# Optimization experiments

Hardware: AMD Instinct MI355X
Metric: run time of the kernel (lower is better)

The kernel has to match this reference:

```python
import jax, jax.numpy as jnp
import numpy as np

B, C1, C2, CF, H, W, NH = 1, 64, 256, 256, 64, 64, 8
HD = CF // NH
EPS = 1e-5


def setup_inputs() -> dict:
    key = jax.random.key(0)
    ks = jax.random.split(key, 12)
    s = 0.02
    return {
        "F_lidar": jax.random.normal(ks[0], (B, C1, H, W), jnp.float32),
        "F_cam": jax.random.normal(ks[1], (B, C2, H, W), jnp.float32),
        "Wq": jax.random.normal(ks[2], (CF, C1), jnp.float32) * s,
        "Wk": jax.random.normal(ks[3], (CF, C2), jnp.float32) * s,
        "Wv": jax.random.normal(ks[4], (CF, C2), jnp.float32) * s,
        "Wo": jax.random.normal(ks[5], (CF, CF), jnp.float32) * s,
        "Wres": jax.random.normal(ks[6], (CF, C1), jnp.float32) * s,
        "ln1_g": jnp.ones((CF,), jnp.float32),
        "ln1_b": jnp.zeros((CF,), jnp.float32),
        "ln2_g": jnp.ones((CF,), jnp.float32),
        "ln2_b": jnp.zeros((CF,), jnp.float32),
        "W1": jax.random.normal(ks[7], (4 * CF, CF), jnp.float32) * s,
        "b1": jnp.zeros((4 * CF,), jnp.float32),
        "W2": jax.random.normal(ks[8], (CF, 4 * CF), jnp.float32) * s,
        "b2": jnp.zeros((CF,), jnp.float32),
    }


def _ln(x, g, b):
    m = jnp.mean(x, axis=-1, keepdims=True)
    v = jnp.mean((x - m) ** 2, axis=-1, keepdims=True)
    return (x - m) * jax.lax.rsqrt(v + EPS) * g + b


def reference(F_lidar, F_cam, Wq, Wk, Wv, Wo, Wres, ln1_g, ln1_b, ln2_g, ln2_b, W1, b1, W2, b2):
    N = H * W
    # 1x1 convs == per-token linear projections on flattened tokens
    tok_l = F_lidar.reshape(B, C1, N).transpose(0, 2, 1)  # (B, N, C1)
    tok_c = F_cam.reshape(B, C2, N).transpose(0, 2, 1)    # (B, N, C2)
    Q = (tok_l @ Wq.T).reshape(B, N, NH, HD)
    K = (tok_c @ Wk.T).reshape(B, N, NH, HD)
    V = (tok_c @ Wv.T).reshape(B, N, NH, HD)
    scale = HD ** -0.5
    scores = jnp.einsum("bnhd,bmhd->bhnm", Q, K) * scale  # (B, NH, N, N)
    attn = jax.nn.softmax(scores, axis=-1)
    out = jnp.einsum("bhnm,bmhd->bnhd", attn, V).reshape(B, N, CF)
    out = out @ Wo.T                                      # out_proj (1x1 conv)
    res = tok_l @ Wres.T                                  # residual_proj
    x = _ln(res + out, ln1_g, ln1_b)
    # FFN (dropout is identity in eval)
    h = jax.nn.relu(x @ W1.T + b1)
    ffn = h @ W2.T + b2
    x = _ln(x + ffn, ln2_g, ln2_b)
    return x.transpose(0, 2, 1).reshape(B, CF, H, W)
```

## Files before the change

### kernel.cpp

```cpp
#include <hip/hip_runtime.h>
#include <math.h>

#define NTOK 4096
#define C1 64
#define C2 256
#define CF 256
#define NH 8
#define HD 32
#define CFF 1024
#define EPSF 1e-5f
#define SPLIT 4
#define KVBLK 128
#define QSCALE 0.25505654040876564f

using f32x4  = __attribute__((ext_vector_type(4))) float;
using bf16x8 = __attribute__((ext_vector_type(8))) short;
using u32x4  = __attribute__((ext_vector_type(4))) unsigned int;
typedef unsigned short ushort_t;

__device__ inline ushort_t f2bf(float x) {
    union { float f; unsigned int u; } v; v.f = x;
    unsigned int r = (v.u + 0x7FFFu + ((v.u >> 16) & 1u)) >> 16;
    return (ushort_t)r;
}
__device__ inline float bf2f(ushort_t u) {
    union { unsigned int i; float f; } v; v.i = ((unsigned int)u) << 16; return v.f;
}
__device__ inline unsigned int fbits(float x) {
    union { float f; unsigned int u; } v; v.f = x; return v.u;
}

__device__ inline float exp2_raw(float x) {
#if __has_builtin(__builtin_amdgcn_exp2f)
    return __builtin_amdgcn_exp2f(x);
#else
    float r;
    asm("v_exp_f32 %0, %1" : "=v"(r) : "v"(x));
    return r;
#endif
}

__global__ __launch_bounds__(256) void prep_kernel(
    const float* __restrict__ Wq, const float* __restrict__ Wk,
    const float* __restrict__ Wv, const float* __restrict__ Wo,
    const float* __restrict__ Wres, const float* __restrict__ W1,
    const float* __restrict__ W2, const float* __restrict__ F_lidar,
    const float* __restrict__ F_cam,
    ushort_t* oWq, ushort_t* oWk, ushort_t* oWv, ushort_t* oWo,
    ushort_t* oWres, ushort_t* oW1, ushort_t* oW2,
    ushort_t* __restrict__ Flt, ushort_t* __restrict__ Fct) {
    __shared__ float tls[32][33];
    int b = blockIdx.x;
    if (b < 736) {
        const float* src; ushort_t* dst; int base, lgK; bool tiled;
        if      (b < 16)  { src = Wq;   dst = oWq;   base = b;       lgK = 6;  tiled = false; }
        else if (b < 80)  { src = Wk;   dst = oWk;   base = b - 16;  lgK = 8;  tiled = false; }
        else if (b < 144) { src = Wv;   dst = oWv;   base = b - 80;  lgK = 8;  tiled = false; }
        else if (b < 208) { src = Wo;   dst = oWo;   base = b - 144; lgK = 8;  tiled = true; }
        else if (b < 224) { src = Wres; dst = oWres; base = b - 208; lgK = 6;  tiled = true; }
        else if (b < 480) { src = W1;   dst = oW1;   base = b - 224; lgK = 8;  tiled = true; }
        else              { src = W2;   dst = oW2;   base = b - 480; lgK = 10; tiled = true; }
        const int i = base * 1024 + threadIdx.x * 4;
        const float4 v = *(const float4*)(src + i);
        ushort4 pk;
        pk.x = f2bf(v.x); pk.y = f2bf(v.y); pk.z = f2bf(v.z); pk.w = f2bf(v.w);
        if (!tiled) {
            *(ushort4*)(dst + i) = pk;
        } else {
            const int c  = i >> lgK;
            const int kk = i & ((1 << lgK) - 1);
            const int tau = (c >> 8) * (1 << (lgK - 6)) + (kk >> 6);
            const int dst4 = tau * 16384 + (c & 255) * 64
                           + (((((kk >> 3) & 7)) ^ (c & 7)) << 3) + (kk & 7);
            *(ushort4*)(dst + dst4) = pk;
        }
        return;
    }
    b -= 736;
    const float* src; ushort_t* dst; int C, c0, n0;
    if (b < 256) { src = F_lidar; dst = Flt; C = C1; c0 = (b & 1) * 32; n0 = (b >> 1) * 32; }
    else { b -= 256; src = F_cam; dst = Fct; C = C2; c0 = (b & 7) * 32; n0 = (b >> 3) * 32; }
    const int tx = threadIdx.x & 31, ty = threadIdx.x >> 5;
#pragma unroll
    for (int i = 0; i < 32; i += 8) tls[ty + i][tx] = src[(size_t)(c0 + ty + i) * NTOK + n0 + tx];
    __syncthreads();
#pragma unroll
    for (int i = 0; i < 32; i += 8) dst[(size_t)(n0 + ty + i) * C + c0 + tx] = f2bf(tls[tx][ty + i]);
}

__global__ __launch_bounds__(256) void qkv_kernel(
    const ushort_t* __restrict__ Flt, const ushort_t* __restrict__ Fct,
    const ushort_t* __restrict__ Wqb, const ushort_t* __restrict__ Wkb,
    const ushort_t* __restrict__ Wvb,
    ushort_t* __restrict__ Qb, ushort_t* __restrict__ Kb, ushort_t* __restrict__ Vt) {
    const int z = blockIdx.z;
    const ushort_t* A = (z == 0) ? Flt : Fct;
    const ushort_t* W = (z == 0) ? Wqb : (z == 1) ? Wkb : Wvb;
    const int K = (z == 0) ? C1 : C2;

    const int tid = threadIdx.x;
    const int wid = tid >> 6, lane = tid & 63;
    const int g = lane >> 4, r = lane & 15;
    const int r0 = blockIdx.x * 128 + wid * 16;
    const int c0 = blockIdx.y * 64;

    f32x4 acc[2][4];
#pragma unroll
    for (int i = 0; i < 2; ++i)
#pragma unroll
        for (int t = 0; t < 4; ++t) acc[i][t] = (f32x4){0, 0, 0, 0};

    const ushort_t* ap0 = A + (size_t)(r0 + r) * K + (g << 3);
    const ushort_t* ap1 = ap0 + (size_t)64 * K;
    const ushort_t* wp = W + (size_t)(c0 + r) * K + (g << 3);
#pragma unroll 2
    for (int k0 = 0; k0 < K; k0 += 32) {
        const bf16x8 a0 = *(const bf16x8*)(ap0 + k0);
        const bf16x8 a1 = *(const bf16x8*)(ap1 + k0);
#pragma unroll
        for (int t = 0; t < 4; ++t) {
            const bf16x8 wf = *(const bf16x8*)(wp + (size_t)(t * 16) * K + k0);
            acc[0][t] = __builtin_amdgcn_mfma_f32_16x16x32_bf16(a0, wf, acc[0][t], 0, 0, 0);
            acc[1][t] = __builtin_amdgcn_mfma_f32_16x16x32_bf16(a1, wf, acc[1][t], 0, 0, 0);
        }
    }
    if (z == 0) {
#pragma unroll
        for (int i = 0; i < 2; ++i)
#pragma unroll
            for (int t = 0; t < 4; ++t) {
                const int col = c0 + 16 * t + r;
#pragma unroll
                for (int q = 0; q < 4; ++q)
                    Qb[(size_t)(r0 + i * 64 + 4 * g + q) * CF + col] = f2bf(acc[i][t][q] * QSCALE);
            }
    } else if (z == 1) {
#pragma unroll
        for (int i = 0; i < 2; ++i)
#pragma unroll
            for (int t = 0; t < 4; ++t) {
                const int col = c0 + 16 * t + r;
#pragma unroll
                for (int q = 0; q < 4; ++q) {
                    const int tok = r0 + i * 64 + 4 * g + q;
                    const int cs = (col & ~31) | ((((col >> 3) & 3) ^ ((tok >> 1) & 3)) << 3) | (col & 7);
                    Kb[(size_t)tok * CF + cs] = f2bf(acc[i][t][q]);
                }
            }
    } else {
#pragma unroll
        for (int i = 0; i < 2; ++i)
#pragma unroll
            for (int t = 0; t < 4; ++t) {
                const int dglob = c0 + 16 * t + r;
                const int hh = dglob >> 5, d = dglob & 31;
                const int tok0 = r0 + i * 64 + 4 * g;
                const int T = tok0 >> 7, tl = tok0 & 127;
                const int kc = tl >> 5, gp = (tl >> 2) & 3, jh = (tl >> 4) & 1;
                const int c = kc * 4 + gp;
                ushort4 pk;
                pk.x = f2bf(acc[i][t][0]); pk.y = f2bf(acc[i][t][1]);
                pk.z = f2bf(acc[i][t][2]); pk.w = f2bf(acc[i][t][3]);
                *(ushort4*)((char*)Vt + ((size_t)(hh * 32 + T) << 13)
                            + ((size_t)(c * 32 + (d ^ (c & 7))) << 4) + (jh << 3)) = pk;
            }
    }
}

__global__ __launch_bounds__(512, 4) void fattn_kernel(const ushort_t* __restrict__ Qb,
                                                       const ushort_t* __restrict__ Kb,
                                                       const ushort_t* __restrict__ Vt,
                                                       ushort_t* __restrict__ Opart,
                                                       float* __restrict__ Lst) {
    __shared__ ushort_t Ks[3][4096];
    __shared__ ushort_t Vs[3][4096];

    const int tid = threadIdx.x;
    const int wid = tid >> 6, lane = tid & 63;
    const int g = lane >> 4, r = lane & 15;
    const int bid = blockIdx.x;
    const int qb = bid & 15;
    const int sp = (bid >> 4) & (SPLIT - 1);
    const int h  = bid >> 6;
    const int n0 = qb * 256 + wid * 32;
    const int m_beg = sp * (NTOK / SPLIT);

    const bf16x8 qfA = *(const bf16x8*)(Qb + ((size_t)(n0 + r) << 8) + h * HD + (g << 3));
    const bf16x8 qfB = *(const bf16x8*)(Qb + ((size_t)(n0 + 16 + r) << 8) + h * HD + (g << 3));
    const bf16x8 onesf = {(short)0x3F80, (short)0x3F80, (short)0x3F80, (short)0x3F80,
                          (short)0x3F80, (short)0x3F80, (short)0x3F80, (short)0x3F80};

    const char* kb  = (const char*)Ks[0] + (r << 6) + ((g ^ ((r >> 1) & 3)) << 4);
    const char* vbg = (const char*)Vs[0] + (g << 9) + ((r & 8) << 4);
    const int slotbase = ((r & 7) ^ g) << 4;

    const int o = tid << 4;
    const char* ksrc = (const char*)Kb + (size_t)(m_beg + (o >> 6)) * 512 + (h << 6) + (o & 63);
    const char* vsrc = (const char*)Vt + ((size_t)(h * 32 + (m_beg >> 7)) << 13) + o;

    auto stage = [&](int bufs) {
        __builtin_amdgcn_global_load_lds(
            (const __attribute__((address_space(1))) unsigned int*)ksrc,
            (__attribute__((address_space(3))) unsigned int*)((char*)Ks[bufs] + (wid << 10)), 16, 0, 0);
        __builtin_amdgcn_global_load_lds(
            (const __attribute__((address_space(1))) unsigned int*)vsrc,
            (__attribute__((address_space(3))) unsigned int*)((char*)Vs[bufs] + (wid << 10)), 16, 0, 0);
        ksrc += KVBLK * 512;
        vsrc += 8192;
    };

    f32x4 accA0 = {0, 0, 0, 0}, accA1 = {0, 0, 0, 0}, laccA = {0, 0, 0, 0};
    f32x4 accB0 = {0, 0, 0, 0}, accB1 = {0, 0, 0, 0}, laccB = {0, 0, 0, 0};

    stage(0);
    stage(1);
    asm volatile("s_waitcnt vmcnt(2)" ::: "memory");
    __builtin_amdgcn_s_barrier();

    constexpr int NT = (NTOK / SPLIT) / KVBLK;
#pragma unroll
    for (int tt = 0; tt < NT; ++tt) {
        if (tt + 2 < NT) stage((tt + 2) % 3);
        const int bofs = (tt % 3) << 13;

        f32x4 sA[8], sB[8];
#pragma unroll
        for (int t8 = 0; t8 < 8; ++t8) {
            const bf16x8 kf = *(const bf16x8*)(kb + bofs + (t8 << 10));
            sA[t8] = __builtin_amdgcn_mfma_f32_16x16x32_bf16(kf, qfA, (f32x4){0, 0, 0, 0}, 0, 0, 0);
            sB[t8] = __builtin_amdgcn_mfma_f32_16x16x32_bf16(kf, qfB, (f32x4){0, 0, 0, 0}, 0, 0, 0);
        }
        u32x4 pkvA[4], pkvB[4];
#pragma unroll
        for (int t8 = 0; t8 < 8; ++t8) {
            const float a0 = exp2_raw(sA[t8][0]);
            const float a1 = exp2_raw(sA[t8][1]);
            const float a2 = exp2_raw(sA[t8][2]);
            const float a3 = exp2_raw(sA[t8][3]);
            pkvA[t8 >> 1][(t8 & 1) * 2]     = __builtin_amdgcn_perm(fbits(a1), fbits(a0), 0x07060302u);
            pkvA[t8 >> 1][(t8 & 1) * 2 + 1] = __builtin_amdgcn_perm(fbits(a3), fbits(a2), 0x07060302u);
        }
#pragma unroll
        for (int t8 = 0; t8 < 8; ++t8) {
            const float b0 = exp2_raw(sB[t8][0]);
            const float b1 = exp2_raw(sB[t8][1]);
            const float b2 = exp2_raw(sB[t8][2]);
            const float b3 = exp2_raw(sB[t8][3]);
            pkvB[t8 >> 1][(t8 & 1) * 2]     = __builtin_amdgcn_perm(fbits(b1), fbits(b0), 0x07060302u);
            pkvB[t8 >> 1][(t8 & 1) * 2 + 1] = __builtin_amdgcn_perm(fbits(b3), fbits(b2), 0x07060302u);
        }
#pragma unroll
        for (int kc = 0; kc < 4; ++kc) {
            union { u32x4 u; bf16x8 b; } puA, puB;
            puA.u = pkvA[kc]; puB.u = pkvB[kc];
            const bf16x8 pfA = puA.b, pfB = puB.b;
            laccA = __builtin_amdgcn_mfma_f32_16x16x32_bf16(pfA, onesf, laccA, 0, 0, 0);
            laccB = __builtin_amdgcn_mfma_f32_16x16x32_bf16(pfB, onesf, laccB, 0, 0, 0);
            const char* va = vbg + bofs + (kc << 11) + (slotbase ^ ((kc & 1) << 6));
            const bf16x8 vf0 = *(const bf16x8*)(va);
            const bf16x8 vf1 = *(const bf16x8*)(va + 256);
            accA0 = __builtin_amdgcn_mfma_f32_16x16x32_bf16(pfA, vf0, accA0, 0, 0, 0);
            accB0 = __builtin_amdgcn_mfma_f32_16x16x32_bf16(pfB, vf0, accB0, 0, 0, 0);
            accA1 = __builtin_amdgcn_mfma_f32_16x16x32_bf16(pfA, vf1, accA1, 0, 0, 0);
            accB1 = __builtin_amdgcn_mfma_f32_16x16x32_bf16(pfB, vf1, accB1, 0, 0, 0);
        }
        if (tt + 2 < NT) { asm volatile("s_waitcnt vmcnt(2)" ::: "memory"); }
        else             { asm volatile("s_waitcnt vmcnt(0)" ::: "memory"); }
        __builtin_amdgcn_s_barrier();
    }
    const size_t baseA = (size_t)(sp * NH + h) * NTOK + n0;
    const size_t baseB = baseA + 16;
    if (r == 0) {
        *(f32x4*)(Lst + baseA + 4 * g) = laccA;
        *(f32x4*)(Lst + baseB + 4 * g) = laccB;
    }
#pragma unroll
    for (int q = 0; q < 4; ++q) {
        const size_t rowbA = (baseA + 4 * g + q) * HD;
        Opart[rowbA + r]      = f2bf(accA0[q]);
        Opart[rowbA + 16 + r] = f2bf(accA1[q]);
        const size_t rowbB = (baseB + 4 * g + q) * HD;
        Opart[rowbB + r]      = f2bf(accB0[q]);
        Opart[rowbB + 16 + r] = f2bf(accB1[q]);
    }
}

__global__ __launch_bounds__(512) void tail_kernel(
    const ushort_t* __restrict__ Opart, const float* __restrict__ Lst,
    const ushort_t* __restrict__ Wo,
    const ushort_t* __restrict__ Flt, const ushort_t* __restrict__ Wres,
    const float* __restrict__ g1, const float* __restrict__ bt1,
    const ushort_t* __restrict__ W1, const float* __restrict__ b1,
    const ushort_t* __restrict__ W2, const float* __restrict__ b2,
    const float* __restrict__ g2, const float* __restrict__ bt2,
    float* __restrict__ out) {
    __shared__ ushort_t Wb[3][16384];
    __shared__ ushort_t As[16][264];
    __shared__ ushort_t Xs[16][264];
    __shared__ ushort_t Hs[16][1032];
    __shared__ float redS[8][16], redQ[8][16];
    const int tid = threadIdx.x;
    const int wid = tid >> 6, lane = tid & 63;
    const int g = lane >> 4, r = lane & 15;
    const int row0 = blockIdx.x * 16;
    const int cw = wid * 32;

    const ushort_t* ap2 = Flt + (size_t)(row0 + r) * C1 + (g << 3);
    const bf16x8 afl0 = *(const bf16x8*)(ap2);
    const bf16x8 afl1 = *(const bf16x8*)(ap2 + 32);

    const int wl00 = (cw + r) * 128 + ((g ^ (r & 7)) << 4);
    const int wl01 = wl00 + 2048;
    const int wl10 = (cw + r) * 128 + (((4 + g) ^ (r & 7)) << 4);
    const int wl11 = wl10 + 2048;

    auto stageW = [&](const ushort_t* src, int buf) {
        const char* s = (const char*)src + (tid << 4);
        char* d = (char*)&Wb[buf][0] + (tid << 4);
#pragma unroll
        for (int j = 0; j < 4; ++j) {
            __builtin_amdgcn_global_load_lds(
                (const __attribute__((address_space(1))) unsigned int*)(s + j * 8192),
                (__attribute__((address_space(3))) unsigned int*)(d + j * 8192), 16, 0, 0);
        }
    };

    {
        const int ri = tid >> 5;
        const int cc = (tid & 31) << 3;
        const int h  = cc >> 5, d0 = cc & 31;
        const int n  = row0 + ri;
        float L = 0.f;
#pragma unroll
        for (int s = 0; s < SPLIT; ++s) L += Lst[(size_t)(s * NH + h) * NTOK + n];
        const float invL = 1.f / L;
        float o[8] = {0.f, 0.f, 0.f, 0.f, 0.f, 0.f, 0.f, 0.f};
#pragma unroll
        for (int s = 0; s < SPLIT; ++s) {
            const ushort_t* p = Opart + ((size_t)(s * NH + h) * NTOK + n) * HD + d0;
            const ushort4 a = *(const ushort4*)p;
            const ushort4 b = *(const ushort4*)(p + 4);
            o[0] += bf2f(a.x); o[1] += bf2f(a.y); o[2] += bf2f(a.z); o[3] += bf2f(a.w);
            o[4] += bf2f(b.x); o[5] += bf2f(b.y); o[6] += bf2f(b.z); o[7] += bf2f(b.w);
        }
        ushort4 m0, m1;
        m0.x = f2bf(o[0] * invL); m0.y = f2bf(o[1] * invL);
        m0.z = f2bf(o[2] * invL); m0.w = f2bf(o[3] * invL);
        m1.x = f2bf(o[4] * invL); m1.y = f2bf(o[5] * invL);
        m1.z = f2bf(o[6] * invL); m1.w = f2bf(o[7] * invL);
        *(ushort4*)&As[ri][cc]     = m0;
        *(ushort4*)&As[ri][cc + 4] = m1;
    }
    __syncthreads();

    f32x4 accB[2] = {{0, 0, 0, 0}, {0, 0, 0, 0}};
    {
        stageW(Wo, 0);
        stageW(Wo + 16384, 1);
        asm volatile("s_waitcnt vmcnt(4)" ::: "memory");
        __builtin_amdgcn_s_barrier();
#pragma unroll
        for (int t = 0; t < 5; ++t) {
            if (t + 2 < 5) stageW(t + 2 < 4 ? Wo + (t + 2) * 16384 : Wres, (t + 2) % 3);
            const char* wb = (const char*)&Wb[t % 3][0];
            const bf16x8 w00 = *(const bf16x8*)(wb + wl00);
            const bf16x8 w01 = *(const bf16x8*)(wb + wl01);
            const bf16x8 w10 = *(const bf16x8*)(wb + wl10);
            const bf16x8 w11 = *(const bf16x8*)(wb + wl11);
            bf16x8 af0, af1;
            if (t < 4) {
                af0 = *(const bf16x8*)&As[r][t * 64 + (g << 3)];
                af1 = *(const bf16x8*)&As[r][t * 64 + 32 + (g << 3)];
            } else {
                af0 = afl0; af1 = afl1;
            }
            accB[0] = __builtin_amdgcn_mfma_f32_16x16x32_bf16(af0, w00, accB[0], 0, 0, 0);
            accB[1] = __builtin_amdgcn_mfma_f32_16x16x32_bf16(af0, w01, accB[1], 0, 0, 0);
            accB[0] = __builtin_amdgcn_mfma_f32_16x16x32_bf16(af1, w10, accB[0], 0, 0, 0);
            accB[1] = __builtin_amdgcn_mfma_f32_16x16x32_bf16(af1, w11, accB[1], 0, 0, 0);
            if (t + 2 < 5) { asm volatile("s_waitcnt vmcnt(4)" ::: "memory"); }
            else           { asm volatile("s_waitcnt vmcnt(0)" ::: "memory"); }
            __builtin_amdgcn_s_barrier();
        }
    }
    f32x4 xv[2];
    {
        f32x4 sv, qv;
#pragma unroll
        for (int q = 0; q < 4; ++q) {
            float s = accB[0][q] + accB[1][q];
            float sq = fmaf(accB[0][q], accB[0][q], accB[1][q] * accB[1][q]);
            s += __shfl_xor(s, 1); s += __shfl_xor(s, 2); s += __shfl_xor(s, 4); s += __shfl_xor(s, 8);
            sq += __shfl_xor(sq, 1); sq += __shfl_xor(sq, 2); sq += __shfl_xor(sq, 4); sq += __shfl_xor(sq, 8);
            sv[q] = s; qv[q] = sq;
        }
        if (r == 0) { *(f32x4*)&redS[wid][4 * g] = sv; *(f32x4*)&redQ[wid][4 * g] = qv; }
        __syncthreads();
        f32x4 S = {0, 0, 0, 0}, SQ = {0, 0, 0, 0};
#pragma unroll
        for (int w = 0; w < 8; ++w) {
            S  += *(const f32x4*)&redS[w][4 * g];
            SQ += *(const f32x4*)&redQ[w][4 * g];
        }
        f32x4 mn4, rs4;
#pragma unroll
        for (int q = 0; q < 4; ++q) {
            mn4[q] = S[q] * (1.f / CF);
            rs4[q] = rsqrtf(fmaxf(SQ[q] * (1.f / CF) - mn4[q] * mn4[q], 0.f) + EPSF);
        }
#pragma unroll
        for (int t = 0; t < 2; ++t) {
            const int col = cw + 16 * t + r;
            const float gam = g1[col], bet = bt1[col];
#pragma unroll
            for (int q = 0; q < 4; ++q) {
                xv[t][q] = (accB[t][q] - mn4[q]) * rs4[q] * gam + bet;
                Xs[4 * g + q][col] = f2bf(xv[t][q]);
            }
        }
    }
    __syncthreads();

    {
        f32x4 acc1[8];
#pragma unroll
        for (int t = 0; t < 8; ++t) acc1[t] = (f32x4){0, 0, 0, 0};
        stageW(W1, 0);
        stageW(W1 + 16384, 1);
        asm volatile("s_waitcnt vmcnt(4)" ::: "memory");
        __builtin_amdgcn_s_barrier();
#pragma unroll
        for (int t = 0; t < 16; ++t) {
            if (t + 2 < 16) stageW(W1 + (size_t)(t + 2) * 16384, (t + 2) % 3);
            const char* wb = (const char*)&Wb[t % 3][0];
            const bf16x8 w00 = *(const bf16x8*)(wb + wl00);
            const bf16x8 w01 = *(const bf16x8*)(wb + wl01);
            const bf16x8 w10 = *(const bf16x8*)(wb + wl10);
            const bf16x8 w11 = *(const bf16x8*)(wb + wl11);
            const bf16x8 af0 = *(const bf16x8*)&Xs[r][(t & 3) * 64 + (g << 3)];
            const bf16x8 af1 = *(const bf16x8*)&Xs[r][(t & 3) * 64 + 32 + (g << 3)];
            const int idx = (t >> 2) * 2;
            acc1[idx]     = __builtin_amdgcn_mfma_f32_16x16x32_bf16(w00, af0, acc1[idx], 0, 0, 0);
            acc1[idx + 1] = __builtin_amdgcn_mfma_f32_16x16x32_bf16(w01, af0, acc1[idx + 1], 0, 0, 0);
            acc1[idx]     = __builtin_amdgcn_mfma_f32_16x16x32_bf16(w10, af1, acc1[idx], 0, 0, 0);
            acc1[idx + 1] = __builtin_amdgcn_mfma_f32_16x16x32_bf16(w11, af1, acc1[idx + 1], 0, 0, 0);
            if (t + 2 < 16) { asm volatile("s_waitcnt vmcnt(4)" ::: "memory"); }
            else            { asm volatile("s_waitcnt vmcnt(0)" ::: "memory"); }
            __builtin_amdgcn_s_barrier();
        }
#pragma unroll
        for (int idx = 0; idx < 8; ++idx) {
            const int colb = (idx >> 1) * 256 + cw + 16 * (idx & 1) + 4 * g;
            const f32x4 bv = *(const f32x4*)(b1 + colb);
            ushort4 hw;
            hw.x = f2bf(fmaxf(acc1[idx][0] + bv[0], 0.f));
            hw.y = f2bf(fmaxf(acc1[idx][1] + bv[1], 0.f));
            hw.z = f2bf(fmaxf(acc1[idx][2] + bv[2], 0.f));
            hw.w = f2bf(fmaxf(acc1[idx][3] + bv[3], 0.f));
            *(ushort4*)&Hs[r][colb] = hw;
        }
    }

    f32x4 accD[2] = {{0, 0, 0, 0}, {0, 0, 0, 0}};
    {
        stageW(W2, 0);
        stageW(W2 + 16384, 1);
        asm volatile("s_waitcnt vmcnt(4)" ::: "memory");
        __builtin_amdgcn_s_barrier();
#pragma unroll
        for (int t = 0; t < 16; ++t) {
            if (t + 2 < 16) stageW(W2 + (size_t)(t + 2) * 16384, (t + 2) % 3);
            const char* wb = (const char*)&Wb[t % 3][0];
            const bf16x8 w00 = *(const bf16x8*)(wb + wl00);
            const bf16x8 w01 = *(const bf16x8*)(wb + wl01);
            const bf16x8 w10 = *(const bf16x8*)(wb + wl10);
            const bf16x8 w11 = *(const bf16x8*)(wb + wl11);
            const bf16x8 af0 = *(const bf16x8*)&Hs[r][t * 64 + (g << 3)];
            const bf16x8 af1 = *(const bf16x8*)&Hs[r][t * 64 + 32 + (g << 3)];
            accD[0] = __builtin_amdgcn_mfma_f32_16x16x32_bf16(af0, w00, accD[0], 0, 0, 0);
            accD[1] = __builtin_amdgcn_mfma_f32_16x16x32_bf16(af0, w01, accD[1], 0, 0, 0);
            accD[0] = __builtin_amdgcn_mfma_f32_16x16x32_bf16(af1, w10, accD[0], 0, 0, 0);
            accD[1] = __builtin_amdgcn_mfma_f32_16x16x32_bf16(af1, w11, accD[1], 0, 0, 0);
            if (t + 2 < 16) { asm volatile("s_waitcnt vmcnt(4)" ::: "memory"); }
            else            { asm volatile("s_waitcnt vmcnt(0)" ::: "memory"); }
            __builtin_amdgcn_s_barrier();
        }
    }
    {
#pragma unroll
        for (int t = 0; t < 2; ++t) {
            const float bb = b2[cw + 16 * t + r];
#pragma unroll
            for (int q = 0; q < 4; ++q) accD[t][q] += bb + xv[t][q];
        }
        f32x4 sv, qv;
#pragma unroll
        for (int q = 0; q < 4; ++q) {
            float s = accD[0][q] + accD[1][q];
            float sq = fmaf(accD[0][q], accD[0][q], accD[1][q] * accD[1][q]);
            s += __shfl_xor(s, 1); s += __shfl_xor(s, 2); s += __shfl_xor(s, 4); s += __shfl_xor(s, 8);
            sq += __shfl_xor(sq, 1); sq += __shfl_xor(sq, 2); sq += __shfl_xor(sq, 4); sq += __shfl_xor(sq, 8);
            sv[q] = s; qv[q] = sq;
        }
        if (r == 0) { *(f32x4*)&redS[wid][4 * g] = sv; *(f32x4*)&redQ[wid][4 * g] = qv; }
        __syncthreads();
        f32x4 S = {0, 0, 0, 0}, SQ = {0, 0, 0, 0};
#pragma unroll
        for (int w = 0; w < 8; ++w) {
            S  += *(const f32x4*)&redS[w][4 * g];
            SQ += *(const f32x4*)&redQ[w][4 * g];
        }
        f32x4 mn4, rs4;
#pragma unroll
        for (int q = 0; q < 4; ++q) {
            mn4[q] = S[q] * (1.f / CF);
            rs4[q] = rsqrtf(fmaxf(SQ[q] * (1.f / CF) - mn4[q] * mn4[q], 0.f) + EPSF);
        }
#pragma unroll
        for (int t = 0; t < 2; ++t) {
            const int col = cw + 16 * t + r;
            const float gam = g2[col], bet = bt2[col];
            f32x4 ov;
#pragma unroll
            for (int q = 0; q < 4; ++q)
                ov[q] = (accD[t][q] - mn4[q]) * rs4[q] * gam + bet;
            *(f32x4*)(out + (size_t)col * NTOK + row0 + 4 * g) = ov;
        }
    }
}

extern "C" void kernel_launch(void* const* d_in, const int* in_sizes, int n_in,
                              void* d_out, int out_size, void* d_ws, size_t ws_size,
                              hipStream_t stream) {
    const float* F_lidar = (const float*)d_in[0];
    const float* F_cam   = (const float*)d_in[1];
    const float* Wq      = (const float*)d_in[2];
    const float* Wk      = (const float*)d_in[3];
    const float* Wv      = (const float*)d_in[4];
    const float* Wo      = (const float*)d_in[5];
    const float* Wres    = (const float*)d_in[6];
    const float* ln1_g   = (const float*)d_in[7];
    const float* ln1_b   = (const float*)d_in[8];
    const float* ln2_g   = (const float*)d_in[9];
    const float* ln2_b   = (const float*)d_in[10];
    const float* W1      = (const float*)d_in[11];
    const float* b1      = (const float*)d_in[12];
    const float* W2      = (const float*)d_in[13];
    const float* b2      = (const float*)d_in[14];
    float* out = (float*)d_out;
    char* ws = (char*)d_ws;

    const size_t KB = 1024, MB = 1024 * 1024;
    ushort_t* Wq_b   = (ushort_t*)(ws + 0);
    ushort_t* Wk_b   = (ushort_t*)(ws + 32 * KB);
    ushort_t* Wv_b   = (ushort_t*)(ws + 160 * KB);
    ushort_t* Wo_b   = (ushort_t*)(ws + 288 * KB);
    ushort_t* Wres_b = (ushort_t*)(ws + 416 * KB);
    ushort_t* W1_b   = (ushort_t*)(ws + 448 * KB);
    ushort_t* W2_b   = (ushort_t*)(ws + 960 * KB);
    ushort_t* Flt    = (ushort_t*)(ws + 1536 * KB);
    ushort_t* Fct    = (ushort_t*)(ws + 2 * MB);
    ushort_t* Qb     = (ushort_t*)(ws + 4 * MB);
    ushort_t* Kb     = (ushort_t*)(ws + 6 * MB);
    ushort_t* Vt     = (ushort_t*)(ws + 8 * MB);
    ushort_t* Opart  = (ushort_t*)(ws + 12 * MB);
    float*    Lst    = (float*)(ws + 20 * MB);

    prep_kernel<<<2016, 256, 0, stream>>>(Wq, Wk, Wv, Wo, Wres, W1, W2, F_lidar, F_cam,
                                          Wq_b, Wk_b, Wv_b, Wo_b, Wres_b, W1_b, W2_b, Flt, Fct);
    qkv_kernel<<<dim3(NTOK / 128, CF / 64, 3), 256, 0, stream>>>(Flt, Fct, Wq_b, Wk_b, Wv_b, Qb, Kb, Vt);
    fattn_kernel<<<NH * SPLIT * (NTOK / 256), 512, 0, stream>>>(Qb, Kb, Vt, Opart, Lst);
    tail_kernel<<<NTOK / 16, 512, 0, stream>>>(Opart, Lst, Wo_b, Flt, Wres_b, ln1_g, ln1_b,
                                               W1_b, b1, W2_b, b2, ln2_g, ln2_b, out);
}
```

Baseline: 68.03 us.

## Unify tail weight streaming into one continuous pipeline and add MFMA priority hints

The tail kernel now streams Wo, Wres, W1 and W2 through a single triple-buffered LDS pipeline indexed by a global stage counter. Weight loads for the next GEMM are prefetched while the previous GEMM and its layernorm epilogue run, which removes the pipeline drain and refill between phases. LayerNorm and bias vectors and the lidar tile are also staged into LDS up front, and the attention kernel wraps its MFMA sections with s_setprio so waves issuing matrix work get scheduling priority. The cost is more LDS use per block and an extra __syncthreads between the FFN phases.

```diff
diff --git a/kernel.cpp b/kernel.cpp
--- a/kernel.cpp
+++ b/kernel.cpp
@@ -224,12 +224,14 @@
         const int bofs = (tt % 3) << 13;
 
         f32x4 sA[8], sB[8];
+        __builtin_amdgcn_s_setprio(1);
 #pragma unroll
         for (int t8 = 0; t8 < 8; ++t8) {
             const bf16x8 kf = *(const bf16x8*)(kb + bofs + (t8 << 10));
             sA[t8] = __builtin_amdgcn_mfma_f32_16x16x32_bf16(kf, qfA, (f32x4){0, 0, 0, 0}, 0, 0, 0);
             sB[t8] = __builtin_amdgcn_mfma_f32_16x16x32_bf16(kf, qfB, (f32x4){0, 0, 0, 0}, 0, 0, 0);
         }
+        __builtin_amdgcn_s_setprio(0);
         u32x4 pkvA[4], pkvB[4];
 #pragma unroll
         for (int t8 = 0; t8 < 8; ++t8) {
@@ -249,6 +251,7 @@
             pkvB[t8 >> 1][(t8 & 1) * 2]     = __builtin_amdgcn_perm(fbits(b1), fbits(b0), 0x07060302u);
             pkvB[t8 >> 1][(t8 & 1) * 2 + 1] = __builtin_amdgcn_perm(fbits(b3), fbits(b2), 0x07060302u);
         }
+        __builtin_amdgcn_s_setprio(1);
 #pragma unroll
         for (int kc = 0; kc < 4; ++kc) {
             union { u32x4 u; bf16x8 b; } puA, puB;
@@ -264,6 +267,7 @@
             accA1 = __builtin_amdgcn_mfma_f32_16x16x32_bf16(pfA, vf1, accA1, 0, 0, 0);
             accB1 = __builtin_amdgcn_mfma_f32_16x16x32_bf16(pfB, vf1, accB1, 0, 0, 0);
         }
+        __builtin_amdgcn_s_setprio(0);
         if (tt + 2 < NT) { asm volatile("s_waitcnt vmcnt(2)" ::: "memory"); }
         else             { asm volatile("s_waitcnt vmcnt(0)" ::: "memory"); }
         __builtin_amdgcn_s_barrier();
@@ -298,6 +302,8 @@
     __shared__ ushort_t As[16][264];
     __shared__ ushort_t Xs[16][264];
     __shared__ ushort_t Hs[16][1032];
+    __shared__ ushort_t Fs[16][72];
+    __shared__ float Bias[2304];
     __shared__ float redS[8][16], redQ[8][16];
     const int tid = threadIdx.x;
     const int wid = tid >> 6, lane = tid & 63;
@@ -305,10 +311,6 @@
     const int row0 = blockIdx.x * 16;
     const int cw = wid * 32;
 
-    const ushort_t* ap2 = Flt + (size_t)(row0 + r) * C1 + (g << 3);
-    const bf16x8 afl0 = *(const bf16x8*)(ap2);
-    const bf16x8 afl1 = *(const bf16x8*)(ap2 + 32);
-
     const int wl00 = (cw + r) * 128 + ((g ^ (r & 7)) << 4);
     const int wl01 = wl00 + 2048;
     const int wl10 = (cw + r) * 128 + (((4 + g) ^ (r & 7)) << 4);
@@ -323,6 +325,12 @@
                 (const __attribute__((address_space(1))) unsigned int*)(s + j * 8192),
                 (__attribute__((address_space(3))) unsigned int*)(d + j * 8192), 16, 0, 0);
         }
+    };
+    auto wsrc = [&](int s) -> const ushort_t* {
+        if (s < 4)  return Wo + (size_t)s * 16384;
+        if (s == 4) return Wres;
+        if (s < 21) return W1 + (size_t)(s - 5) * 16384;
+        return W2 + (size_t)(s - 21) * 16384;
     };
 
     {
@@ -350,38 +358,53 @@
         m1.z = f2bf(o[6] * invL); m1.w = f2bf(o[7] * invL);
         *(ushort4*)&As[ri][cc]     = m0;
         *(ushort4*)&As[ri][cc + 4] = m1;
+        *(ushort2*)&Fs[ri][(tid & 31) * 2] =
+            *(const ushort2*)(Flt + (size_t)(row0 + ri) * C1 + (tid & 31) * 2);
+#pragma unroll
+        for (int i5 = 0; i5 < 5; ++i5) {
+            const int i = i5 * 512 + tid;
+            if (i < 2304) {
+                float v;
+                if      (i < 256)  v = g1[i];
+                else if (i < 512)  v = bt1[i - 256];
+                else if (i < 768)  v = b2[i - 512];
+                else if (i < 1024) v = g2[i - 768];
+                else if (i < 1280) v = bt2[i - 1024];
+                else               v = b1[i - 1280];
+                Bias[i] = v;
+            }
+        }
     }
     __syncthreads();
 
+    stageW(wsrc(0), 0);
+    stageW(wsrc(1), 1);
+    asm volatile("s_waitcnt vmcnt(4)" ::: "memory");
+    __builtin_amdgcn_s_barrier();
+
     f32x4 accB[2] = {{0, 0, 0, 0}, {0, 0, 0, 0}};
-    {
-        stageW(Wo, 0);
-        stageW(Wo + 16384, 1);
+#pragma unroll
+    for (int t = 0; t < 5; ++t) {
+        stageW(wsrc(t + 2), (t + 2) % 3);
+        const char* wb = (const char*)&Wb[t % 3][0];
+        const bf16x8 w00 = *(const bf16x8*)(wb + wl00);
+        const bf16x8 w01 = *(const bf16x8*)(wb + wl01);
+        const bf16x8 w10 = *(const bf16x8*)(wb + wl10);
+        const bf16x8 w11 = *(const bf16x8*)(wb + wl11);
+        bf16x8 af0, af1;
+        if (t < 4) {
+            af0 = *(const bf16x8*)&As[r][t * 64 + (g << 3)];
+            af1 = *(const bf16x8*)&As[r][t * 64 + 32 + (g << 3)];
+        } else {
+            af0 = *(const bf16x8*)&Fs[r][(g << 3)];
+            af1 = *(const bf16x8*)&Fs[r][32 + (g << 3)];
+        }
+        accB[0] = __builtin_amdgcn_mfma_f32_16x16x32_bf16(af0, w00, accB[0], 0, 0, 0);
+        accB[1] = __builtin_amdgcn_mfma_f32_16x16x32_bf16(af0, w01, accB[1], 0, 0, 0);
+        accB[0] = __builtin_amdgcn_mfma_f32_16x16x32_bf16(af1, w10, accB[0], 0, 0, 0);
+        accB[1] = __builtin_amdgcn_mfma_f32_16x16x32_bf16(af1, w11, accB[1], 0, 0, 0);
         asm volatile("s_waitcnt vmcnt(4)" ::: "memory");
         __builtin_amdgcn_s_barrier();
-#pragma unroll
-        for (int t = 0; t < 5; ++t) {
-            if (t + 2 < 5) stageW(t + 2 < 4 ? Wo + (t + 2) * 16384 : Wres, (t + 2) % 3);
-            const char* wb = (const char*)&Wb[t % 3][0];
-            const bf16x8 w00 = *(const bf16x8*)(wb + wl00);
-            const bf16x8 w01 = *(const bf16x8*)(wb + wl01);
-            const bf16x8 w10 = *(const bf16x8*)(wb + wl10);
-            const bf16x8 w11 = *(const bf16x8*)(wb + wl11);
-            bf16x8 af0, af1;
-            if (t < 4) {
-                af0 = *(const bf16x8*)&As[r][t * 64 + (g << 3)];
-                af1 = *(const bf16x8*)&As[r][t * 64 + 32 + (g << 3)];
-            } else {
-                af0 = afl0; af1 = afl1;
-            }
-            accB[0] = __builtin_amdgcn_mfma_f32_16x16x32_bf16(af0, w00, accB[0], 0, 0, 0);
-            accB[1] = __builtin_amdgcn_mfma_f32_16x16x32_bf16(af0, w01, accB[1], 0, 0, 0);
-            accB[0] = __builtin_amdgcn_mfma_f32_16x16x32_bf16(af1, w10, accB[0], 0, 0, 0);
-            accB[1] = __builtin_amdgcn_mfma_f32_16x16x32_bf16(af1, w11, accB[1], 0, 0, 0);
-            if (t + 2 < 5) { asm volatile("s_waitcnt vmcnt(4)" ::: "memory"); }
-            else           { asm volatile("s_waitcnt vmcnt(0)" ::: "memory"); }
-            __builtin_amdgcn_s_barrier();
-        }
     }
     f32x4 xv[2];
     {
@@ -411,7 +434,7 @@
 #pragma unroll
         for (int t = 0; t < 2; ++t) {
             const int col = cw + 16 * t + r;
-            const float gam = g1[col], bet = bt1[col];
+            const float gam = Bias[col], bet = Bias[256 + col];
 #pragma unroll
             for (int q = 0; q < 4; ++q) {
                 xv[t][q] = (accB[t][q] - mn4[q]) * rs4[q] * gam + bet;
@@ -425,33 +448,29 @@
         f32x4 acc1[8];
 #pragma unroll
         for (int t = 0; t < 8; ++t) acc1[t] = (f32x4){0, 0, 0, 0};
-        stageW(W1, 0);
-        stageW(W1 + 16384, 1);
-        asm volatile("s_waitcnt vmcnt(4)" ::: "memory");
-        __builtin_amdgcn_s_barrier();
-#pragma unroll
-        for (int t = 0; t < 16; ++t) {
-            if (t + 2 < 16) stageW(W1 + (size_t)(t + 2) * 16384, (t + 2) % 3);
+#pragma unroll
+        for (int t = 5; t < 21; ++t) {
+            stageW(wsrc(t + 2), (t + 2) % 3);
+            const int tc = t - 5;
             const char* wb = (const char*)&Wb[t % 3][0];
             const bf16x8 w00 = *(const bf16x8*)(wb + wl00);
             const bf16x8 w01 = *(const bf16x8*)(wb + wl01);
             const bf16x8 w10 = *(const bf16x8*)(wb + wl10);
             const bf16x8 w11 = *(const bf16x8*)(wb + wl11);
-            const bf16x8 af0 = *(const bf16x8*)&Xs[r][(t & 3) * 64 + (g << 3)];
-            const bf16x8 af1 = *(const bf16x8*)&Xs[r][(t & 3) * 64 + 32 + (g << 3)];
-            const int idx = (t >> 2) * 2;
+            const bf16x8 af0 = *(const bf16x8*)&Xs[r][(tc & 3) * 64 + (g << 3)];
+            const bf16x8 af1 = *(const bf16x8*)&Xs[r][(tc & 3) * 64 + 32 + (g << 3)];
+            const int idx = (tc >> 2) * 2;
             acc1[idx]     = __builtin_amdgcn_mfma_f32_16x16x32_bf16(w00, af0, acc1[idx], 0, 0, 0);
             acc1[idx + 1] = __builtin_amdgcn_mfma_f32_16x16x32_bf16(w01, af0, acc1[idx + 1], 0, 0, 0);
             acc1[idx]     = __builtin_amdgcn_mfma_f32_16x16x32_bf16(w10, af1, acc1[idx], 0, 0, 0);
             acc1[idx + 1] = __builtin_amdgcn_mfma_f32_16x16x32_bf16(w11, af1, acc1[idx + 1], 0, 0, 0);
-            if (t + 2 < 16) { asm volatile("s_waitcnt vmcnt(4)" ::: "memory"); }
-            else            { asm volatile("s_waitcnt vmcnt(0)" ::: "memory"); }
+            asm volatile("s_waitcnt vmcnt(4)" ::: "memory");
             __builtin_amdgcn_s_barrier();
         }
 #pragma unroll
         for (int idx = 0; idx < 8; ++idx) {
             const int colb = (idx >> 1) * 256 + cw + 16 * (idx & 1) + 4 * g;
-            const f32x4 bv = *(const f32x4*)(b1 + colb);
+            const f32x4 bv = *(const f32x4*)&Bias[1280 + colb];
             ushort4 hw;
             hw.x = f2bf(fmaxf(acc1[idx][0] + bv[0], 0.f));
             hw.y = f2bf(fmaxf(acc1[idx][1] + bv[1], 0.f));
@@ -460,36 +479,32 @@
             *(ushort4*)&Hs[r][colb] = hw;
         }
     }
+    __syncthreads();
 
     f32x4 accD[2] = {{0, 0, 0, 0}, {0, 0, 0, 0}};
+#pragma unroll
+    for (int t = 21; t < 37; ++t) {
+        if (t + 2 < 37) stageW(wsrc(t + 2), (t + 2) % 3);
+        const int tc = t - 21;
+        const char* wb = (const char*)&Wb[t % 3][0];
+        const bf16x8 w00 = *(const bf16x8*)(wb + wl00);
+        const bf16x8 w01 = *(const bf16x8*)(wb + wl01);
+        const bf16x8 w10 = *(const bf16x8*)(wb + wl10);
+        const bf16x8 w11 = *(const bf16x8*)(wb + wl11);
+        const bf16x8 af0 = *(const bf16x8*)&Hs[r][tc * 64 + (g << 3)];
+        const bf16x8 af1 = *(const bf16x8*)&Hs[r][tc * 64 + 32 + (g << 3)];
+        accD[0] = __builtin_amdgcn_mfma_f32_16x16x32_bf16(af0, w00, accD[0], 0, 0, 0);
+        accD[1] = __builtin_amdgcn_mfma_f32_16x16x32_bf16(af0, w01, accD[1], 0, 0, 0);
+        accD[0] = __builtin_amdgcn_mfma_f32_16x16x32_bf16(af1, w10, accD[0], 0, 0, 0);
+        accD[1] = __builtin_amdgcn_mfma_f32_16x16x32_bf16(af1, w11, accD[1], 0, 0, 0);
+        if (t + 2 < 37) { asm volatile("s_waitcnt vmcnt(4)" ::: "memory"); }
+        else            { asm volatile("s_waitcnt vmcnt(0)" ::: "memory"); }
+        __builtin_amdgcn_s_barrier();
+    }
     {
-        stageW(W2, 0);
-        stageW(W2 + 16384, 1);
-        asm volatile("s_waitcnt vmcnt(4)" ::: "memory");
-        __builtin_amdgcn_s_barrier();
-#pragma unroll
-        for (int t = 0; t < 16; ++t) {
-            if (t + 2 < 16) stageW(W2 + (size_t)(t + 2) * 16384, (t + 2) % 3);
-            const char* wb = (const char*)&Wb[t % 3][0];
-            const bf16x8 w00 = *(const bf16x8*)(wb + wl00);
-            const bf16x8 w01 = *(const bf16x8*)(wb + wl01);
-            const bf16x8 w10 = *(const bf16x8*)(wb + wl10);
-            const bf16x8 w11 = *(const bf16x8*)(wb + wl11);
-            const bf16x8 af0 = *(const bf16x8*)&Hs[r][t * 64 + (g << 3)];
-            const bf16x8 af1 = *(const bf16x8*)&Hs[r][t * 64 + 32 + (g << 3)];
-            accD[0] = __builtin_amdgcn_mfma_f32_16x16x32_bf16(af0, w00, accD[0], 0, 0, 0);
-            accD[1] = __builtin_amdgcn_mfma_f32_16x16x32_bf16(af0, w01, accD[1], 0, 0, 0);
-            accD[0] = __builtin_amdgcn_mfma_f32_16x16x32_bf16(af1, w10, accD[0], 0, 0, 0);
-            accD[1] = __builtin_amdgcn_mfma_f32_16x16x32_bf16(af1, w11, accD[1], 0, 0, 0);
-            if (t + 2 < 16) { asm volatile("s_waitcnt vmcnt(4)" ::: "memory"); }
-            else            { asm volatile("s_waitcnt vmcnt(0)" ::: "memory"); }
-            __builtin_amdgcn_s_barrier();
-        }
-    }
-    {
 #pragma unroll
         for (int t = 0; t < 2; ++t) {
-            const float bb = b2[cw + 16 * t + r];
+            const float bb = Bias[512 + cw + 16 * t + r];
 #pragma unroll
             for (int q = 0; q < 4; ++q) accD[t][q] += bb + xv[t][q];
         }
@@ -519,7 +534,7 @@
 #pragma unroll
         for (int t = 0; t < 2; ++t) {
             const int col = cw + 16 * t + r;
-            const float gam = g2[col], bet = bt2[col];
+            const float gam = Bias[768 + col], bet = Bias[1024 + col];
             f32x4 ov;
 #pragma unroll
             for (int q = 0; q < 4; ++q)
```

After: 69.58 us. +2.3%, slower.
